# Performance work log

Measured on AMD Instinct MI355X. Metric: run time of the kernel, lower is better.

Reference implementation:

```python
import jax, jax.numpy as jnp
import numpy as np

BITS = 8
K = 2 ** BITS          # number of clusters
KMEANS_ITERS = 10      # fixed Lloyd iterations (stand-in for fit_predict convergence)


def _kmeans_1d(x_flat, key):
    """1-D euclidean k-means on x_flat [N]. Returns (labels [N] int32, centers [K])."""
    n = x_flat.shape[0]
    # init: random sample of data points (fast-pytorch-kmeans style)
    init_idx = jax.random.randint(key, (K,), 0, n)
    centers0 = x_flat[init_idx]

    def assign(centers):
        # |x - c| has same argmin as (x - c)^2 in 1-D
        d = jnp.abs(x_flat[:, None] - centers[None, :])  # [N, K]
        return jnp.argmin(d, axis=1)                      # [N]

    def body(_, centers):
        labels = assign(centers)
        sums = jax.ops.segment_sum(x_flat, labels, num_segments=K)
        counts = jax.ops.segment_sum(jnp.ones_like(x_flat), labels, num_segments=K)
        # keep old center for empty clusters
        return jnp.where(counts > 0, sums / jnp.maximum(counts, 1.0), centers)

    centers = jax.lax.fori_loop(0, KMEANS_ITERS, body, centers0)
    labels = assign(centers)
    return labels, centers


def setup_inputs() -> dict:
    key = jax.random.key(0)
    x = jax.random.normal(key, (4, 512, 1024), dtype=jnp.float32)
    return {"input": x}


def reference(input) -> jnp.ndarray:
    shape = input.shape
    x_flat = input.reshape(-1)
    labels, centers = _kmeans_1d(x_flat, jax.random.key(42))
    # fused label -> center remap (single gather instead of 2^bits masked writes)
    out = centers[labels].reshape(shape)
    return out
```

## Files before the change

kernel.cpp:

```cpp
#include <hip/hip_runtime.h>
#include <stdint.h>

#define NPTS (1u << 21)
#define KC 256
#define KM_ITERS 10
#define CHUNK 4096
#define NCHUNK (NPTS / CHUNK)

__device__ __forceinline__ uint32_t rotl32(uint32_t v, uint32_t s) {
  return (v << s) | (v >> (32u - s));
}

__device__ void threefry2x32_key(uint32_t k0, uint32_t k1,
                                 uint32_t c0, uint32_t c1,
                                 uint32_t* o0, uint32_t* o1) {
  uint32_t ks[3] = {k0, k1, k0 ^ k1 ^ 0x1BD11BDAu};
  uint32_t x0 = c0 + ks[0];
  uint32_t x1 = c1 + ks[1];
  const uint32_t rotA[4] = {13u, 15u, 26u, 6u};
  const uint32_t rotB[4] = {17u, 29u, 16u, 24u};
  #pragma unroll
  for (int i = 0; i < 5; ++i) {
    const uint32_t* rot = ((i & 1) == 0) ? rotA : rotB;
    #pragma unroll
    for (int r = 0; r < 4; ++r) {
      x0 += x1;
      x1 = rotl32(x1, rot[r]);
      x1 ^= x0;
    }
    x0 += ks[(i + 1) % 3];
    x1 += ks[(i + 2) % 3] + (uint32_t)(i + 1);
  }
  *o0 = x0;
  *o1 = x1;
}

__global__ void km_init(const float* __restrict__ x, float* __restrict__ centers) {
  int j = threadIdx.x;
  uint32_t s0, s1;
  threefry2x32_key(0u, 42u, 0u, 1u, &s0, &s1);
  uint32_t b0, b1;
  threefry2x32_key(s0, s1, 0u, (uint32_t)j, &b0, &b1);
  uint32_t idx = (b0 ^ b1) & (NPTS - 1u);
  centers[j] = x[idx];
}

__global__ __launch_bounds__(256) void km_sort_centers(
    const float* __restrict__ centers, float* __restrict__ sortedC,
    uint32_t* __restrict__ rep) {
  __shared__ float v[KC];
  __shared__ int idx[KC];
  __shared__ uint32_t r[KC];
  const int t = threadIdx.x;
  v[t] = centers[t];
  idx[t] = t;
  __syncthreads();
  for (int size = 2; size <= KC; size <<= 1) {
    for (int stride = size >> 1; stride > 0; stride >>= 1) {
      int partner = t ^ stride;
      if (partner > t) {
        bool ascending = ((t & size) == 0);
        float va = v[t], vb = v[partner];
        int ia = idx[t], ib = idx[partner];
        bool doswap = ascending ? (va > vb) : (va < vb);
        if (doswap) { v[t] = vb; v[partner] = va; idx[t] = ib; idx[partner] = ia; }
      }
      __syncthreads();
    }
  }
  if (t == 0) {
    float cv = v[0];
    uint32_t cur = (uint32_t)idx[0];
    r[0] = cur;
    for (int j = 1; j < KC; ++j) {
      if (v[j] == cv) { uint32_t ij = (uint32_t)idx[j]; cur = (ij < cur) ? ij : cur; }
      else { cv = v[j]; cur = (uint32_t)idx[j]; }
      r[j] = cur;
    }
    float nv = v[KC - 1];
    uint32_t nc = r[KC - 1];
    for (int j = KC - 2; j >= 0; --j) {
      if (v[j] == nv) { nc = (r[j] < nc) ? r[j] : nc; r[j] = nc; }
      else { nv = v[j]; nc = r[j]; }
    }
  }
  __syncthreads();
  sortedC[t] = v[t];
  rep[t] = r[t];
}

__device__ __forceinline__ uint32_t bs_label(float x, const float* sC,
                                             const uint32_t* rp) {
  int pos = 0;
  #pragma unroll
  for (int d = 128; d >= 1; d >>= 1)
    if (sC[pos + d - 1] <= x) pos += d;
  if (pos == 0) return rp[0];
  float cl = sC[pos - 1], cr = sC[pos & 255];
  float dl = fabsf(x - cl), dr = fabsf(x - cr);
  if (dl < dr) return rp[pos - 1];
  if (dr < dl) return rp[pos];
  uint32_t a = rp[pos - 1], b = rp[pos];
  return a < b ? a : b;
}

__global__ __launch_bounds__(256) void km_assign_hist(
    const float* __restrict__ x, const float* __restrict__ sortedC,
    const uint32_t* __restrict__ rep, uint32_t* __restrict__ hist) {
  __shared__ float sC[KC];
  __shared__ uint32_t rp[KC];
  __shared__ uint32_t sH[KC];
  const int t = threadIdx.x, b = blockIdx.x;
  sC[t] = sortedC[t];
  rp[t] = rep[t];
  sH[t] = 0u;
  __syncthreads();

  #pragma unroll
  for (int q = 0; q < 4; ++q) {
    const int i4 = b * (CHUNK / 4) + q * 256 + t;
    float4 xv = reinterpret_cast<const float4*>(x)[i4];
    uint32_t l0 = bs_label(xv.x, sC, rp);
    uint32_t l1 = bs_label(xv.y, sC, rp);
    uint32_t l2 = bs_label(xv.z, sC, rp);
    uint32_t l3 = bs_label(xv.w, sC, rp);
    atomicAdd(&sH[l0], 1u);
    atomicAdd(&sH[l1], 1u);
    atomicAdd(&sH[l2], 1u);
    atomicAdd(&sH[l3], 1u);
  }
  __syncthreads();
  hist[b * KC + t] = sH[t];
}

__global__ __launch_bounds__(512) void km_scan_chunks(
    uint32_t* __restrict__ hist, uint32_t* __restrict__ clusterStart) {
  __shared__ uint32_t s[NCHUNK];
  const int k = blockIdx.x, t = threadIdx.x;
  uint32_t v = hist[t * KC + k];
  s[t] = v;
  __syncthreads();
  #pragma unroll
  for (int d = 1; d < NCHUNK; d <<= 1) {
    uint32_t u = (t >= d) ? s[t - d] : 0u;
    __syncthreads();
    s[t] += u;
    __syncthreads();
  }
  hist[t * KC + k] = s[t] - v;
  if (t == NCHUNK - 1) clusterStart[k] = s[t];
}

__global__ void km_scan_clusters(uint32_t* __restrict__ clusterStart) {
  if (threadIdx.x != 0) return;
  uint32_t acc = 0;
  for (int j = 0; j < KC; ++j) {
    uint32_t t = clusterStart[j];
    clusterStart[j] = acc;
    acc += t;
  }
  clusterStart[KC] = acc;
}

__global__ __launch_bounds__(256) void km_scatter(
    const float* __restrict__ x, const float* __restrict__ sortedC,
    const uint32_t* __restrict__ rep,
    const uint32_t* __restrict__ hist, const uint32_t* __restrict__ clusterStart,
    float* __restrict__ sorted_x) {
  __shared__ float sC[KC];
  __shared__ uint32_t rp[KC];
  __shared__ uint32_t run[KC];
  __shared__ uint32_t cntw[4][KC];
  __shared__ uint32_t basew[4][KC];
  const int t = threadIdx.x, b = blockIdx.x;
  const int w = t >> 6, lane = t & 63;
  sC[t] = sortedC[t];
  rp[t] = rep[t];
  run[t] = hist[b * KC + t] + clusterStart[t];
  __syncthreads();

  for (int r = 0; r < CHUNK / 256; ++r) {
    const int i = b * CHUNK + r * 256 + t;
    const float xv = x[i];
    uint32_t lab = bs_label(xv, sC, rp);
    unsigned long long m = ~0ULL;
    #pragma unroll
    for (int bit = 0; bit < 8; ++bit) {
      unsigned long long vote = __ballot((lab >> bit) & 1u);
      m &= ((lab >> bit) & 1u) ? vote : ~vote;
    }
    uint32_t rank = (uint32_t)__popcll(m & ((1ULL << lane) - 1ULL));
    uint32_t wcnt = (uint32_t)__popcll(m);
    cntw[0][t] = 0u; cntw[1][t] = 0u; cntw[2][t] = 0u; cntw[3][t] = 0u;
    __syncthreads();
    if (rank == 0) cntw[w][lab] = wcnt;
    __syncthreads();
    {
      uint32_t c0 = cntw[0][t], c1 = cntw[1][t], c2 = cntw[2][t], c3 = cntw[3][t];
      uint32_t base = run[t];
      basew[0][t] = base;
      basew[1][t] = base + c0;
      basew[2][t] = base + c0 + c1;
      basew[3][t] = base + c0 + c1 + c2;
      run[t] = base + c0 + c1 + c2 + c3;
    }
    __syncthreads();
    sorted_x[basew[w][lab] + rank] = xv;
  }
}

#define LOADG(p0, p1, p2, p3, p4, p5, p6, p7, base) \
  p0 = b4[(base) + 0]; p1 = b4[(base) + 1];         \
  p2 = b4[(base) + 2]; p3 = b4[(base) + 3];         \
  p4 = b4[(base) + 4]; p5 = b4[(base) + 5];         \
  p6 = b4[(base) + 6]; p7 = b4[(base) + 7];

#define FOLD4(q) s += (q).x; s += (q).y; s += (q).z; s += (q).w;

#define FOLDG(p0, p1, p2, p3, p4, p5, p6, p7) \
  FOLD4(p0) FOLD4(p1) FOLD4(p2) FOLD4(p3)     \
  FOLD4(p4) FOLD4(p5) FOLD4(p6) FOLD4(p7)

__global__ __launch_bounds__(64) void km_fold_update(
    const float* __restrict__ sorted_x, const uint32_t* __restrict__ clusterStart,
    float* __restrict__ centers) {
  __shared__ __align__(16) float buf[2][256];
  const int k = blockIdx.x;
  const uint32_t lane = threadIdx.x;
  const uint32_t s0 = clusterStart[k], s1 = clusterStart[k + 1];
  const uint32_t cnt = s1 - s0;
  const float* p = sorted_x + s0;
  const uint32_t ntiles = (cnt + 255u) >> 8;

  if (ntiles > 0) {
    uint32_t i0 = lane * 4u;
    float4 v = make_float4(0.f, 0.f, 0.f, 0.f);
    if (i0 + 3u < cnt) {
      v = *reinterpret_cast<const float4*>(p + i0);
    } else {
      if (i0 + 0u < cnt) v.x = p[i0 + 0u];
      if (i0 + 1u < cnt) v.y = p[i0 + 1u];
      if (i0 + 2u < cnt) v.z = p[i0 + 2u];
    }
    *reinterpret_cast<float4*>(&buf[0][lane * 4u]) = v;
  }
  __syncthreads();

  float s = 0.0f;
  for (uint32_t t = 0; t < ntiles; ++t) {
    const bool have_next = (t + 1u < ntiles);
    float4 vn = make_float4(0.f, 0.f, 0.f, 0.f);
    if (have_next) {
      uint32_t i0 = (t + 1u) * 256u + lane * 4u;
      if (i0 + 3u < cnt) {
        vn = *reinterpret_cast<const float4*>(p + i0);
      } else {
        if (i0 + 0u < cnt) vn.x = p[i0 + 0u];
        if (i0 + 1u < cnt) vn.y = p[i0 + 1u];
        if (i0 + 2u < cnt) vn.z = p[i0 + 2u];
      }
    }
    if (lane == 0) {
      const float* bb = buf[t & 1u];
      uint32_t m = cnt - t * 256u;
      if (m > 256u) m = 256u;
      if (m == 256u) {
        const float4* b4 = reinterpret_cast<const float4*>(bb);
        float4 a0, a1, a2, a3, a4, a5, a6, a7;
        float4 c0, c1, c2, c3, c4, c5, c6, c7;
        LOADG(a0, a1, a2, a3, a4, a5, a6, a7, 0)
        LOADG(c0, c1, c2, c3, c4, c5, c6, c7, 8)
        FOLDG(a0, a1, a2, a3, a4, a5, a6, a7)
        LOADG(a0, a1, a2, a3, a4, a5, a6, a7, 16)
        FOLDG(c0, c1, c2, c3, c4, c5, c6, c7)
        LOADG(c0, c1, c2, c3, c4, c5, c6, c7, 24)
        FOLDG(a0, a1, a2, a3, a4, a5, a6, a7)
        LOADG(a0, a1, a2, a3, a4, a5, a6, a7, 32)
        FOLDG(c0, c1, c2, c3, c4, c5, c6, c7)
        LOADG(c0, c1, c2, c3, c4, c5, c6, c7, 40)
        FOLDG(a0, a1, a2, a3, a4, a5, a6, a7)
        LOADG(a0, a1, a2, a3, a4, a5, a6, a7, 48)
        FOLDG(c0, c1, c2, c3, c4, c5, c6, c7)
        LOADG(c0, c1, c2, c3, c4, c5, c6, c7, 56)
        FOLDG(a0, a1, a2, a3, a4, a5, a6, a7)
        FOLDG(c0, c1, c2, c3, c4, c5, c6, c7)
      } else {
        uint32_t j = 0;
        for (; j + 16u <= m; j += 16u) {
          float v0 = bb[j + 0], v1 = bb[j + 1], v2 = bb[j + 2], v3 = bb[j + 3];
          float v4 = bb[j + 4], v5 = bb[j + 5], v6 = bb[j + 6], v7 = bb[j + 7];
          float v8 = bb[j + 8], v9 = bb[j + 9], va = bb[j + 10], vb = bb[j + 11];
          float vc = bb[j + 12], vd = bb[j + 13], ve = bb[j + 14], vf = bb[j + 15];
          s += v0; s += v1; s += v2; s += v3;
          s += v4; s += v5; s += v6; s += v7;
          s += v8; s += v9; s += va; s += vb;
          s += vc; s += vd; s += ve; s += vf;
        }
        for (; j < m; ++j) s += bb[j];
      }
    }
    if (have_next) {
      *reinterpret_cast<float4*>(&buf[(t + 1u) & 1u][lane * 4u]) = vn;
    }
    __syncthreads();
  }
  if (lane == 0 && cnt > 0) centers[k] = s / (float)cnt;
}

__global__ __launch_bounds__(256) void km_final(
    const float* __restrict__ x, const float* __restrict__ centers,
    const float* __restrict__ sortedC, const uint32_t* __restrict__ rep,
    float* __restrict__ out) {
  __shared__ float sC[KC];
  __shared__ uint32_t rp[KC];
  __shared__ float sCtr[KC];
  const int t = threadIdx.x;
  sC[t] = sortedC[t];
  rp[t] = rep[t];
  sCtr[t] = centers[t];
  __syncthreads();

  const int nv = (int)(NPTS / 4u);
  for (int i = blockIdx.x * blockDim.x + t; i < nv; i += gridDim.x * blockDim.x) {
    float4 xv = reinterpret_cast<const float4*>(x)[i];
    float4 o;
    o.x = sCtr[bs_label(xv.x, sC, rp)];
    o.y = sCtr[bs_label(xv.y, sC, rp)];
    o.z = sCtr[bs_label(xv.z, sC, rp)];
    o.w = sCtr[bs_label(xv.w, sC, rp)];
    reinterpret_cast<float4*>(out)[i] = o;
  }
}

extern "C" void kernel_launch(void* const* d_in, const int* in_sizes, int n_in,
                              void* d_out, int out_size, void* d_ws, size_t ws_size,
                              hipStream_t stream) {
  const float* x = (const float*)d_in[0];
  float* out = (float*)d_out;

  uint8_t* ws = (uint8_t*)d_ws;
  float* centers = (float*)(ws + 0);
  uint32_t* clusterStart = (uint32_t*)(ws + 1024);
  float* sortedC = (float*)(ws + 2560);
  uint32_t* rep = (uint32_t*)(ws + 3584);
  uint32_t* hist = (uint32_t*)(ws + 8192);
  float* sorted_x = (float*)d_out;

  km_init<<<1, KC, 0, stream>>>(x, centers);
  for (int it = 0; it < KM_ITERS; ++it) {
    km_sort_centers<<<1, KC, 0, stream>>>(centers, sortedC, rep);
    km_assign_hist<<<NCHUNK, 256, 0, stream>>>(x, sortedC, rep, hist);
    km_scan_chunks<<<KC, NCHUNK, 0, stream>>>(hist, clusterStart);
    km_scan_clusters<<<1, 64, 0, stream>>>(clusterStart);
    km_scatter<<<NCHUNK, 256, 0, stream>>>(x, sortedC, rep, hist, clusterStart,
                                           sorted_x);
    km_fold_update<<<KC, 64, 0, stream>>>(sorted_x, clusterStart, centers);
  }
  km_sort_centers<<<1, KC, 0, stream>>>(centers, sortedC, rep);
  km_final<<<1024, 256, 0, stream>>>(x, centers, sortedC, rep, out);
}
```

Measured before the change: 1.861 ms.

## Fold cluster sums straight from global memory with three-deep register prefetch

The per-cluster fold kernel no longer stages tiles through double-buffered shared memory with barriers and a lane-0-only reduction. Every lane now loads uniform-address float4 groups of 64 values directly from global memory into three rotating register banks. Each lane folds one bank in the original sequential order while the next two banks are in flight. This removes the LDS round-trip and the per-tile __syncthreads, and keeps several memory requests outstanding behind the serial add chain. In exchange it uses many registers (launch bounds 64,1), makes every lane do the same redundant work, and clamps out-of-range loads to the end of the buffer.

```diff
diff --git a/kernel.cpp b/kernel.cpp
--- a/kernel.cpp
+++ b/kernel.cpp
@@ -209,102 +209,54 @@
   }
 }
 
-#define LOADG(p0, p1, p2, p3, p4, p5, p6, p7, base) \
-  p0 = b4[(base) + 0]; p1 = b4[(base) + 1];         \
-  p2 = b4[(base) + 2]; p3 = b4[(base) + 3];         \
-  p4 = b4[(base) + 4]; p5 = b4[(base) + 5];         \
-  p6 = b4[(base) + 6]; p7 = b4[(base) + 7];
-
-#define FOLD4(q) s += (q).x; s += (q).y; s += (q).z; s += (q).w;
-
-#define FOLDG(p0, p1, p2, p3, p4, p5, p6, p7) \
-  FOLD4(p0) FOLD4(p1) FOLD4(p2) FOLD4(p3)     \
-  FOLD4(p4) FOLD4(p5) FOLD4(p6) FOLD4(p7)
-
-__global__ __launch_bounds__(64) void km_fold_update(
+#define LDG4(v, g, j) { \
+  uint32_t o_ = s0 + (((uint32_t)(g)) << 6) + ((uint32_t)(j) << 2); \
+  o_ = (o_ > (NPTS - 4u)) ? (NPTS - 4u) : o_; \
+  (v) = *reinterpret_cast<const float4*>(sx + o_); }
+
+#define LOADG64(P, g) \
+  LDG4(P##0, g, 0) LDG4(P##1, g, 1) LDG4(P##2, g, 2) LDG4(P##3, g, 3) \
+  LDG4(P##4, g, 4) LDG4(P##5, g, 5) LDG4(P##6, g, 6) LDG4(P##7, g, 7) \
+  LDG4(P##8, g, 8) LDG4(P##9, g, 9) LDG4(P##10, g, 10) LDG4(P##11, g, 11) \
+  LDG4(P##12, g, 12) LDG4(P##13, g, 13) LDG4(P##14, g, 14) LDG4(P##15, g, 15)
+
+#define F4(q) s += (q).x; s += (q).y; s += (q).z; s += (q).w;
+
+#define FOLDG64(P) \
+  F4(P##0) F4(P##1) F4(P##2) F4(P##3) F4(P##4) F4(P##5) F4(P##6) F4(P##7) \
+  F4(P##8) F4(P##9) F4(P##10) F4(P##11) F4(P##12) F4(P##13) F4(P##14) F4(P##15)
+
+__global__ __launch_bounds__(64, 1) void km_fold_update(
     const float* __restrict__ sorted_x, const uint32_t* __restrict__ clusterStart,
     float* __restrict__ centers) {
-  __shared__ __align__(16) float buf[2][256];
   const int k = blockIdx.x;
-  const uint32_t lane = threadIdx.x;
   const uint32_t s0 = clusterStart[k], s1 = clusterStart[k + 1];
   const uint32_t cnt = s1 - s0;
-  const float* p = sorted_x + s0;
-  const uint32_t ntiles = (cnt + 255u) >> 8;
-
-  if (ntiles > 0) {
-    uint32_t i0 = lane * 4u;
-    float4 v = make_float4(0.f, 0.f, 0.f, 0.f);
-    if (i0 + 3u < cnt) {
-      v = *reinterpret_cast<const float4*>(p + i0);
-    } else {
-      if (i0 + 0u < cnt) v.x = p[i0 + 0u];
-      if (i0 + 1u < cnt) v.y = p[i0 + 1u];
-      if (i0 + 2u < cnt) v.z = p[i0 + 2u];
-    }
-    *reinterpret_cast<float4*>(&buf[0][lane * 4u]) = v;
-  }
-  __syncthreads();
+  const float* sx = sorted_x;
+  const uint32_t nfull = cnt >> 6;
 
   float s = 0.0f;
-  for (uint32_t t = 0; t < ntiles; ++t) {
-    const bool have_next = (t + 1u < ntiles);
-    float4 vn = make_float4(0.f, 0.f, 0.f, 0.f);
-    if (have_next) {
-      uint32_t i0 = (t + 1u) * 256u + lane * 4u;
-      if (i0 + 3u < cnt) {
-        vn = *reinterpret_cast<const float4*>(p + i0);
-      } else {
-        if (i0 + 0u < cnt) vn.x = p[i0 + 0u];
-        if (i0 + 1u < cnt) vn.y = p[i0 + 1u];
-        if (i0 + 2u < cnt) vn.z = p[i0 + 2u];
-      }
-    }
-    if (lane == 0) {
-      const float* bb = buf[t & 1u];
-      uint32_t m = cnt - t * 256u;
-      if (m > 256u) m = 256u;
-      if (m == 256u) {
-        const float4* b4 = reinterpret_cast<const float4*>(bb);
-        float4 a0, a1, a2, a3, a4, a5, a6, a7;
-        float4 c0, c1, c2, c3, c4, c5, c6, c7;
-        LOADG(a0, a1, a2, a3, a4, a5, a6, a7, 0)
-        LOADG(c0, c1, c2, c3, c4, c5, c6, c7, 8)
-        FOLDG(a0, a1, a2, a3, a4, a5, a6, a7)
-        LOADG(a0, a1, a2, a3, a4, a5, a6, a7, 16)
-        FOLDG(c0, c1, c2, c3, c4, c5, c6, c7)
-        LOADG(c0, c1, c2, c3, c4, c5, c6, c7, 24)
-        FOLDG(a0, a1, a2, a3, a4, a5, a6, a7)
-        LOADG(a0, a1, a2, a3, a4, a5, a6, a7, 32)
-        FOLDG(c0, c1, c2, c3, c4, c5, c6, c7)
-        LOADG(c0, c1, c2, c3, c4, c5, c6, c7, 40)
-        FOLDG(a0, a1, a2, a3, a4, a5, a6, a7)
-        LOADG(a0, a1, a2, a3, a4, a5, a6, a7, 48)
-        FOLDG(c0, c1, c2, c3, c4, c5, c6, c7)
-        LOADG(c0, c1, c2, c3, c4, c5, c6, c7, 56)
-        FOLDG(a0, a1, a2, a3, a4, a5, a6, a7)
-        FOLDG(c0, c1, c2, c3, c4, c5, c6, c7)
-      } else {
-        uint32_t j = 0;
-        for (; j + 16u <= m; j += 16u) {
-          float v0 = bb[j + 0], v1 = bb[j + 1], v2 = bb[j + 2], v3 = bb[j + 3];
-          float v4 = bb[j + 4], v5 = bb[j + 5], v6 = bb[j + 6], v7 = bb[j + 7];
-          float v8 = bb[j + 8], v9 = bb[j + 9], va = bb[j + 10], vb = bb[j + 11];
-          float vc = bb[j + 12], vd = bb[j + 13], ve = bb[j + 14], vf = bb[j + 15];
-          s += v0; s += v1; s += v2; s += v3;
-          s += v4; s += v5; s += v6; s += v7;
-          s += v8; s += v9; s += va; s += vb;
-          s += vc; s += vd; s += ve; s += vf;
-        }
-        for (; j < m; ++j) s += bb[j];
-      }
-    }
-    if (have_next) {
-      *reinterpret_cast<float4*>(&buf[(t + 1u) & 1u][lane * 4u]) = vn;
-    }
-    __syncthreads();
-  }
-  if (lane == 0 && cnt > 0) centers[k] = s / (float)cnt;
+  float4 A0, A1, A2, A3, A4, A5, A6, A7, A8, A9, A10, A11, A12, A13, A14, A15;
+  float4 B0, B1, B2, B3, B4, B5, B6, B7, B8, B9, B10, B11, B12, B13, B14, B15;
+  float4 C0, C1, C2, C3, C4, C5, C6, C7, C8, C9, C10, C11, C12, C13, C14, C15;
+
+  LOADG64(A, 0u)
+  LOADG64(B, 1u)
+  LOADG64(C, 2u)
+
+  uint32_t t = 0u;
+  while (t + 3u <= nfull) {
+    FOLDG64(A) LOADG64(A, t + 3u)
+    FOLDG64(B) LOADG64(B, t + 4u)
+    FOLDG64(C) LOADG64(C, t + 5u)
+    t += 3u;
+  }
+  if (t < nfull) { FOLDG64(A) }
+  if (t + 1u < nfull) { FOLDG64(B) }
+
+  for (uint32_t j = nfull << 6; j < cnt; ++j) s += sx[s0 + j];
+
+  if (threadIdx.x == 0 && cnt > 0u) centers[k] = s / (float)cnt;
 }
 
 __global__ __launch_bounds__(256) void km_final(
```

New measurement: 5.788 ms. 3.11x slower.
